# Kernel tuning notes

Measured on AMD Instinct MI355X. Metric: run time of the kernel, lower is better.

Reference implementation:

```python
import jax, jax.numpy as jnp
import numpy as np

T = 2048          # total (flattened) tokens
HID = 4096
NQ = 32           # query heads
NKV = 8           # kv heads
D = 128           # head_dim
B = 4             # dllm block length (block-sparse attention block)
WIN = 1024        # sliding window
EPS = 1e-6


def _rope_tables():
    # standard RoPE cos/sin tables, half-dim frequencies duplicated
    inv_freq = 1.0 / (10000.0 ** (np.arange(0, D, 2, dtype=np.float32) / D))
    pos = np.arange(T, dtype=np.float32)
    freqs = np.outer(pos, inv_freq)                     # [T, D/2]
    emb = np.concatenate([freqs, freqs], axis=-1)       # [T, D]
    return jnp.asarray(np.cos(emb)), jnp.asarray(np.sin(emb))


def setup_inputs() -> dict:
    key = jax.random.key(0)
    ks = jax.random.split(key, 4)
    cos, sin = _rope_tables()
    return {
        "hidden_states": jax.random.normal(ks[0], (T, HID), jnp.float32),
        "cos": cos,
        "sin": sin,
        "w_qkv": jax.random.normal(ks[1], (HID, (NQ + 2 * NKV) * D), jnp.float32) * (HID ** -0.5),
        "q_norm_w": jnp.ones((D,), jnp.float32),
        "k_norm_w": jnp.ones((D,), jnp.float32),
        "w_o": jax.random.normal(ks[2], (NQ * D, HID), jnp.float32) * ((NQ * D) ** -0.5),
    }


def _rmsnorm(x, w):
    # per-head RMSNorm over last dim (head_dim)
    var = jnp.mean(jnp.square(x), axis=-1, keepdims=True)
    return x * jax.lax.rsqrt(var + EPS) * w


def _rotate_half(x):
    x1, x2 = jnp.split(x, 2, axis=-1)
    return jnp.concatenate([-x2, x1], axis=-1)


def reference(hidden_states, cos, sin, w_qkv, q_norm_w, k_norm_w, w_o):
    # fused QKV projection on flattened tokens [T, HID]
    qkv = hidden_states @ w_qkv                                  # [T, (NQ+2NKV)*D]
    q, k, v = jnp.split(qkv, [NQ * D, (NQ + NKV) * D], axis=-1)
    q = q.reshape(T, NQ, D)
    k = k.reshape(T, NKV, D)
    v = v.reshape(T, NKV, D)

    # per-head QK RMSNorm
    q = _rmsnorm(q, q_norm_w)
    k = _rmsnorm(k, k_norm_w)

    # RoPE
    c = cos[:, None, :]
    s = sin[:, None, :]
    q = q * c + _rotate_half(q) * s
    k = k * c + _rotate_half(k) * s

    # GQA: expand kv heads to query heads
    groups = NQ // NKV
    k = jnp.repeat(k, groups, axis=1)                            # [T, NQ, D]
    v = jnp.repeat(v, groups, axis=1)

    # block-sparse (dLLM block-causal) + sliding-window mask:
    # token q attends to token j iff block(j) <= block(q) (full bidirectional
    # attention within a dllm block, causal across blocks) AND j is within
    # the sliding window.
    pos = jnp.arange(T)
    qb = pos // B
    allowed = (qb[None, :] <= qb[:, None]) & ((pos[:, None] - pos[None, :]) < WIN)

    scale = D ** -0.5
    scores = jnp.einsum("qhd,khd->hqk", q, k) * scale            # [NQ, T, T]
    scores = jnp.where(allowed[None, :, :], scores, jnp.float32(-1e30))
    probs = jax.nn.softmax(scores, axis=-1)
    attn = jnp.einsum("hqk,khd->qhd", probs, v)                   # [T, NQ, D]

    out = attn.reshape(T, NQ * D) @ w_o                           # [T, HID]
    return out
```

## Files before the change

### kernel.cpp

```cpp
#include <hip/hip_runtime.h>
#include <hip/hip_bf16.h>

typedef unsigned short u16;
typedef __attribute__((ext_vector_type(8))) short bf16x8;
typedef __attribute__((ext_vector_type(4))) float f32x4;
typedef __attribute__((ext_vector_type(8))) u16 u16x8;
typedef __attribute__((ext_vector_type(4))) u16 u16x4;

#define T_SEQ 2048
#define HID 4096
#define NQ 32
#define NKV 8
#define DH 128
#define WIN 1024

__device__ __forceinline__ u16 f2bf(float f) {
  union { float f; unsigned int u; } v; v.f = f;
  unsigned int u = v.u;
  unsigned int r = (u + 0x7FFFu + ((u >> 16) & 1u)) >> 16;
  return (u16)r;
}
__device__ __forceinline__ float bf2f(u16 b) {
  union { unsigned int u; float f; } v; v.u = ((unsigned int)b) << 16;
  return v.f;
}

__device__ __forceinline__ void gload16(const void* g, void* l) {
  __builtin_amdgcn_global_load_lds(
      (const __attribute__((address_space(1))) unsigned int*)g,
      (__attribute__((address_space(3))) unsigned int*)l, 16, 0, 0);
}

__global__ __launch_bounds__(256) void f32_to_bf16(const float* __restrict__ in,
                                                   u16* __restrict__ out, int n) {
  int i = (blockIdx.x * 256 + threadIdx.x) * 8;
  if (i >= n) return;
  float4 a = *(const float4*)(in + i);
  float4 b = *(const float4*)(in + i + 4);
  u16x8 r;
  r[0] = f2bf(a.x); r[1] = f2bf(a.y); r[2] = f2bf(a.z); r[3] = f2bf(a.w);
  r[4] = f2bf(b.x); r[5] = f2bf(b.y); r[6] = f2bf(b.z); r[7] = f2bf(b.w);
  *(u16x8*)(out + i) = r;
}

__global__ __launch_bounds__(256) void transpose_f32_to_bf16(const float* __restrict__ in,
                                                             u16* __restrict__ out,
                                                             int R, int C) {
  __shared__ float tile[64][65];
  int c0 = blockIdx.x * 64, r0 = blockIdx.y * 64;
  int tx = threadIdx.x, ty = threadIdx.y;
#pragma unroll
  for (int i = 0; i < 64; i += 16) {
    float4 v = *(const float4*)(in + (size_t)(r0 + ty + i) * C + c0 + tx * 4);
    tile[ty + i][tx * 4 + 0] = v.x;
    tile[ty + i][tx * 4 + 1] = v.y;
    tile[ty + i][tx * 4 + 2] = v.z;
    tile[ty + i][tx * 4 + 3] = v.w;
  }
  __syncthreads();
#pragma unroll
  for (int i = 0; i < 64; i += 16) {
    u16x4 o;
#pragma unroll
    for (int j = 0; j < 4; ++j) o[j] = f2bf(tile[tx * 4 + j][ty + i]);
    *(u16x4*)(out + (size_t)(c0 + ty + i) * R + r0 + tx * 4) = o;
  }
}

__global__ __launch_bounds__(256) void v_transpose(const u16* __restrict__ Vn,
                                                   u16* __restrict__ Vt) {
  __shared__ u16 tile[64][68];
  int tx = threadIdx.x & 15, ty = threadIdx.x >> 4;
  int t0 = blockIdx.x * 64, dh0 = blockIdx.y * 64;
#pragma unroll
  for (int i = 0; i < 64; i += 16) {
    u16x4 v = *(const u16x4*)(Vn + (size_t)(t0 + ty + i) * 1024 + dh0 + tx * 4);
    tile[ty + i][tx * 4 + 0] = v[0];
    tile[ty + i][tx * 4 + 1] = v[1];
    tile[ty + i][tx * 4 + 2] = v[2];
    tile[ty + i][tx * 4 + 3] = v[3];
  }
  __syncthreads();
#pragma unroll
  for (int i = 0; i < 64; i += 16) {
    u16x4 o;
#pragma unroll
    for (int j = 0; j < 4; ++j) o[j] = tile[tx * 4 + j][ty + i];
    *(u16x4*)(Vt + (size_t)(dh0 + ty + i) * 2048 + t0 + tx * 4) = o;
  }
}

template <int NF, bool BF16OUT>
__global__ __launch_bounds__(512, 2) void gemm_1w(const u16* __restrict__ A,
                                                  const u16* __restrict__ Bt,
                                                  void* __restrict__ Cv,
                                                  int N, int K, int NT) {
  constexpr int HN = NF * 16;
  constexpr int BN = 4 * HN;
  constexpr int NB = BN / 64;
  __shared__ u16 lsA[2][16384];
  __shared__ u16 lsB[3][BN * 64];
  const int tid = threadIdx.x;
  const int lane = tid & 63, w = tid >> 6;
  const int wm = w >> 1, wn = w & 1;
  const int l15 = lane & 15, l4 = lane >> 4;

  const int nwg = gridDim.x;
  const int cpx = nwg >> 3;
  const int bid = blockIdx.x;
  const int swz = (bid & 7) * cpx + (bid >> 3);
  const int bm = (swz & 7) * 256;
  const int bn = (swz >> 3) * BN;

  auto stageA = [&](int unit, int slot, int kt) {
    int r = tid >> 3, cp = tid & 7;
    int scp = cp ^ (r & 7);
    gload16(A + (size_t)(bm + unit * 64 + r) * K + kt * 64 + scp * 8,
            (char*)lsA[slot] + (unit * 512 + tid) * 16);
  };
  auto stageB = [&](int unit, int slot, int kt) {
    int r = tid >> 3, cp = tid & 7;
    int scp = cp ^ (r & 7);
    gload16(Bt + (size_t)(bn + unit * 64 + r) * K + kt * 64 + scp * 8,
            (char*)lsB[slot] + (unit * 512 + tid) * 16);
  };
  auto rdA = [&](int slot, int mf, int ks) -> bf16x8 {
    int r = wm * 64 + mf * 16 + l15;
    int ch = (ks * 4 + l4) ^ (r & 7);
    return *(const bf16x8*)(lsA[slot] + r * 64 + ch * 8);
  };
  auto rdB = [&](int slot, int nf, int ks) -> bf16x8 {
    int r = wn * 2 * HN + nf * 16 + l15;
    int ch = (ks * 4 + l4) ^ (r & 7);
    return *(const bf16x8*)(lsB[slot] + r * 64 + ch * 8);
  };

#define WAIT_NB() do { if constexpr (NB == 3) asm volatile("s_waitcnt vmcnt(3)" ::: "memory"); \
                       else                   asm volatile("s_waitcnt vmcnt(2)" ::: "memory"); } while (0)

  f32x4 acc[4][2 * NF] = {};
  bf16x8 afA[4][2], bfr[2 * NF][2];

  stageA(0, 0, 0); stageA(1, 0, 0); stageA(2, 0, 0); stageA(3, 0, 0);
#pragma unroll
  for (int u = 0; u < NB; ++u) stageB(u, 0, 0);
#pragma unroll
  for (int u = 0; u < NB; ++u) stageB(u, 1, 1);
  WAIT_NB();
  __builtin_amdgcn_s_barrier();

  for (int t = 0; t < NT; ++t) {
    const int sA = t & 1, sB = t % 3;
    const int ktA = (t + 1 < NT) ? t + 1 : NT - 1;
    const int ktB = (t + 2 < NT) ? t + 2 : NT - 1;

#pragma unroll
    for (int mf = 0; mf < 4; ++mf)
#pragma unroll
      for (int ks = 0; ks < 2; ++ks) afA[mf][ks] = rdA(sA, mf, ks);
#pragma unroll
    for (int nf = 0; nf < 2 * NF; ++nf)
#pragma unroll
      for (int ks = 0; ks < 2; ++ks) bfr[nf][ks] = rdB(sB, nf, ks);
    stageA(0, (t + 1) & 1, ktA); stageA(1, (t + 1) & 1, ktA);
    stageA(2, (t + 1) & 1, ktA); stageA(3, (t + 1) & 1, ktA);
#pragma unroll
    for (int u = 0; u < NB; ++u) stageB(u, (t + 2) % 3, ktB);
    __builtin_amdgcn_s_setprio(1);
#pragma unroll
    for (int nf = 0; nf < 2 * NF; ++nf)
#pragma unroll
      for (int mf = 0; mf < 4; ++mf) {
        acc[mf][nf] = __builtin_amdgcn_mfma_f32_16x16x32_bf16(afA[mf][0], bfr[nf][0], acc[mf][nf], 0, 0, 0);
        acc[mf][nf] = __builtin_amdgcn_mfma_f32_16x16x32_bf16(afA[mf][1], bfr[nf][1], acc[mf][nf], 0, 0, 0);
      }
    __builtin_amdgcn_s_setprio(0);
    asm volatile("s_waitcnt lgkmcnt(0)" ::: "memory");
    WAIT_NB();
    __builtin_amdgcn_s_barrier();
  }

  asm volatile("s_waitcnt vmcnt(0)" ::: "memory");

#pragma unroll
  for (int mi = 0; mi < 4; ++mi)
#pragma unroll
    for (int ni = 0; ni < 2 * NF; ++ni) {
      int row = bm + wm * 64 + mi * 16 + l4 * 4;
      int col = bn + wn * 2 * HN + ni * 16 + l15;
      if constexpr (BF16OUT) {
        u16* dst = (u16*)Cv;
#pragma unroll
        for (int j = 0; j < 4; ++j)
          dst[(size_t)(row + j) * N + col] = f2bf(acc[mi][ni][j]);
      } else {
        float* p = (float*)Cv + (size_t)row * N + col;
        p[0] = acc[mi][ni][0];
        p[(size_t)N] = acc[mi][ni][1];
        p[2 * (size_t)N] = acc[mi][ni][2];
        p[3 * (size_t)N] = acc[mi][ni][3];
      }
    }
#undef WAIT_NB
}

__global__ __launch_bounds__(256, 2) void gemm_1wh(const u16* __restrict__ A,
                                                   const u16* __restrict__ Bt,
                                                   float* __restrict__ C,
                                                   int N, int K, int NT) {
  __shared__ u16 lsA[2][8192];
  __shared__ u16 lsB[3][8192];
  const int tid = threadIdx.x;
  const int lane = tid & 63, w = tid >> 6;
  const int wm = w >> 1, wn = w & 1;
  const int l15 = lane & 15, l4 = lane >> 4;

  const int nwg = gridDim.x;
  const int cpx = nwg >> 3;
  const int bid = blockIdx.x;
  const int swz = (bid & 7) * cpx + (bid >> 3);
  const int bm = (swz & 15) * 128;
  const int bn = (swz >> 4) * 128;

  auto stageA = [&](int unit, int slot, int kt) {
    int r = unit * 32 + (tid >> 3), cp = tid & 7;
    int scp = cp ^ (r & 7);
    gload16(A + (size_t)(bm + r) * K + kt * 64 + scp * 8,
            (char*)lsA[slot] + (unit * 256 + tid) * 16);
  };
  auto stageB = [&](int unit, int slot, int kt) {
    int r = unit * 32 + (tid >> 3), cp = tid & 7;
    int scp = cp ^ (r & 7);
    gload16(Bt + (size_t)(bn + r) * K + kt * 64 + scp * 8,
            (char*)lsB[slot] + (unit * 256 + tid) * 16);
  };
  auto rdA = [&](int slot, int mf, int ks) -> bf16x8 {
    int r = wm * 64 + mf * 16 + l15;
    int ch = (ks * 4 + l4) ^ (r & 7);
    return *(const bf16x8*)(lsA[slot] + r * 64 + ch * 8);
  };
  auto rdB = [&](int slot, int nf, int ks) -> bf16x8 {
    int r = wn * 64 + nf * 16 + l15;
    int ch = (ks * 4 + l4) ^ (r & 7);
    return *(const bf16x8*)(lsB[slot] + r * 64 + ch * 8);
  };

  f32x4 acc[4][4] = {};
  bf16x8 afA[4][2], bfr[4][2];

#pragma unroll
  for (int u = 0; u < 4; ++u) stageA(u, 0, 0);
#pragma unroll
  for (int u = 0; u < 4; ++u) stageB(u, 0, 0);
#pragma unroll
  for (int u = 0; u < 4; ++u) stageB(u, 1, 1);
  asm volatile("s_waitcnt vmcnt(4)" ::: "memory");
  __builtin_amdgcn_s_barrier();

  for (int t = 0; t < NT; ++t) {
    const int sA = t & 1, sB = t % 3;
    const int ktA = (t + 1 < NT) ? t + 1 : NT - 1;
    const int ktB = (t + 2 < NT) ? t + 2 : NT - 1;

#pragma unroll
    for (int mf = 0; mf < 4; ++mf)
#pragma unroll
      for (int ks = 0; ks < 2; ++ks) afA[mf][ks] = rdA(sA, mf, ks);
#pragma unroll
    for (int nf = 0; nf < 4; ++nf)
#pragma unroll
      for (int ks = 0; ks < 2; ++ks) bfr[nf][ks] = rdB(sB, nf, ks);
#pragma unroll
    for (int u = 0; u < 4; ++u) stageA(u, (t + 1) & 1, ktA);
#pragma unroll
    for (int u = 0; u < 4; ++u) stageB(u, (t + 2) % 3, ktB);
    __builtin_amdgcn_s_setprio(1);
#pragma unroll
    for (int nf = 0; nf < 4; ++nf)
#pragma unroll
      for (int mf = 0; mf < 4; ++mf) {
        acc[mf][nf] = __builtin_amdgcn_mfma_f32_16x16x32_bf16(afA[mf][0], bfr[nf][0], acc[mf][nf], 0, 0, 0);
        acc[mf][nf] = __builtin_amdgcn_mfma_f32_16x16x32_bf16(afA[mf][1], bfr[nf][1], acc[mf][nf], 0, 0, 0);
      }
    __builtin_amdgcn_s_setprio(0);
    asm volatile("s_waitcnt lgkmcnt(0)" ::: "memory");
    asm volatile("s_waitcnt vmcnt(4)" ::: "memory");
    __builtin_amdgcn_s_barrier();
  }

  asm volatile("s_waitcnt vmcnt(0)" ::: "memory");

#pragma unroll
  for (int mi = 0; mi < 4; ++mi)
#pragma unroll
    for (int ni = 0; ni < 4; ++ni) {
      int row = bm + wm * 64 + mi * 16 + l4 * 4;
      int col = bn + wn * 64 + ni * 16 + l15;
      float* p = C + (size_t)row * N + col;
      p[0] = acc[mi][ni][0];
      p[(size_t)N] = acc[mi][ni][1];
      p[2 * (size_t)N] = acc[mi][ni][2];
      p[3 * (size_t)N] = acc[mi][ni][3];
    }
}

__global__ __launch_bounds__(256) void rope_kernel(const u16* __restrict__ qkv,
                                                   const float* __restrict__ cosb,
                                                   const float* __restrict__ sinb,
                                                   const float* __restrict__ qw,
                                                   const float* __restrict__ kw,
                                                   u16* __restrict__ Qo,
                                                   u16* __restrict__ Ko,
                                                   u16* __restrict__ Vn) {
  const int tid = threadIdx.x;
  const int v = blockIdx.x * 16 + (tid >> 4);
  const int j = tid & 15;
  const int t = v / 48, hid = v % 48;
  u16x8 raw = *(const u16x8*)(qkv + (size_t)v * 128 + j * 8);
  if (hid < NQ + NKV) {
    float xf[8];
    float ss = 0.f;
#pragma unroll
    for (int i = 0; i < 8; ++i) { xf[i] = bf2f(raw[i]); ss += xf[i] * xf[i]; }
    ss += __shfl_xor(ss, 1); ss += __shfl_xor(ss, 2);
    ss += __shfl_xor(ss, 4); ss += __shfl_xor(ss, 8);
    float inv = rsqrtf(ss * (1.0f / 128.0f) + 1e-6f);
    const float* wn = (hid < NQ) ? qw : kw;
    float4 w0 = *(const float4*)(wn + j * 8);
    float4 w1 = *(const float4*)(wn + j * 8 + 4);
    float wv[8] = {w0.x, w0.y, w0.z, w0.w, w1.x, w1.y, w1.z, w1.w};
    float n[8], p[8];
#pragma unroll
    for (int i = 0; i < 8; ++i) n[i] = xf[i] * inv * wv[i];
#pragma unroll
    for (int i = 0; i < 8; ++i) p[i] = __shfl_xor(n[i], 8);
    const float sgn = (j < 8) ? -1.f : 1.f;
    const float* cb = cosb + t * 128 + j * 8;
    const float* sb = sinb + t * 128 + j * 8;
    float4 c0 = *(const float4*)cb, c1 = *(const float4*)(cb + 4);
    float4 s0 = *(const float4*)sb, s1 = *(const float4*)(sb + 4);
    float cc[8] = {c0.x, c0.y, c0.z, c0.w, c1.x, c1.y, c1.z, c1.w};
    float sv[8] = {s0.x, s0.y, s0.z, s0.w, s1.x, s1.y, s1.z, s1.w};
    const float scale = (hid < NQ) ? 0.08838834764831845f * 1.44269504088896341f : 1.0f;
    u16x8 o;
#pragma unroll
    for (int i = 0; i < 8; ++i)
      o[i] = f2bf((n[i] * cc[i] + sgn * p[i] * sv[i]) * scale);
    if (hid < NQ)
      *(u16x8*)(Qo + ((size_t)hid * T_SEQ + t) * 128 + j * 8) = o;
    else
      *(u16x8*)(Ko + ((size_t)(hid - NQ) * T_SEQ + t) * 128 + j * 8) = o;
  } else {
    *(u16x8*)(Vn + (size_t)t * 1024 + (hid - (NQ + NKV)) * 128 + j * 8) = raw;
  }
}

__global__ __launch_bounds__(256) void attn_kernel(const u16* __restrict__ Q,
                                                   const u16* __restrict__ Kb,
                                                   const u16* __restrict__ Vt,
                                                   u16* __restrict__ O) {
  __shared__ u16 kls[2][64 * 128];
  __shared__ u16 vls[2][128 * 64];
  __shared__ u16 plds[4][16 * 72];

  const int tid = threadIdx.x;
  const int lane = tid & 63, w = tid >> 6;
  const int l15 = lane & 15, l4 = lane >> 4;
  const int h = blockIdx.x;
  const int q0 = blockIdx.y * 64;
  const int wq0 = q0 + w * 16;
  const int kvh = h >> 2;

  bf16x8 qf[4];
  {
    const u16* qrow = Q + ((size_t)h * T_SEQ + (wq0 + l15)) * DH;
    for (int ks = 0; ks < 4; ++ks)
      qf[ks] = *(const bf16x8*)(qrow + ks * 32 + l4 * 8);
  }

  f32x4 acc[8] = {};
  float m = -1e30f, lsum = 0.f;

  int ks0 = q0 - (WIN - 1); if (ks0 < 0) ks0 = 0;
  ks0 &= ~63;
  const int kend = q0;

  auto stage = [&](int b, int k0) {
#pragma unroll
    for (int c = 0; c < 4; ++c) {
      int base = w * 4096 + c * 1024;
      int idx = base / 16 + lane;
      {
        int row = idx >> 4;
        int col = (idx & 15) ^ (row & 7);
        gload16(Kb + ((size_t)kvh * T_SEQ + k0 + row) * DH + col * 8,
                (char*)kls[b] + base);
      }
      {
        int d = idx >> 3;
        int ch = (idx & 7) ^ (d & 7);
        gload16(Vt + ((size_t)kvh * DH + d) * T_SEQ + k0 + ch * 8,
                (char*)vls[b] + base);
      }
    }
  };

  stage(0, ks0);
  int buf = 0;
  for (int k0 = ks0; k0 <= kend; k0 += 64) {
    bool more = (k0 + 64 <= kend);
    if (more) stage(buf ^ 1, k0 + 64);
    if (more) { asm volatile("s_waitcnt vmcnt(8)" ::: "memory"); }
    else      { asm volatile("s_waitcnt vmcnt(0)" ::: "memory"); }
    __builtin_amdgcn_s_barrier();

    if (k0 <= wq0 + 15 && k0 + 63 >= wq0 - (WIN - 1)) {
      f32x4 st[4];
      __builtin_amdgcn_s_setprio(1);
#pragma unroll
      for (int kh = 0; kh < 4; ++kh) {
        f32x4 s = {};
        int row = kh * 16 + l15;
        const char* kb = (const char*)kls[buf] + row * 256;
#pragma unroll
        for (int ks = 0; ks < 4; ++ks) {
          int chunk = (ks * 4 + l4) ^ (row & 7);
          bf16x8 kf = *(const bf16x8*)(kb + chunk * 16);
          s = __builtin_amdgcn_mfma_f32_16x16x32_bf16(kf, qf[ks], s, 0, 0, 0);
        }
        st[kh] = s;
      }
      __builtin_amdgcn_s_setprio(0);
      const int q = wq0 + l15;
      float pv[4][4];
      float mx = -3e38f;
      if (k0 + 64 <= wq0 && k0 >= wq0 - 1008) {
#pragma unroll
        for (int kh = 0; kh < 4; ++kh)
#pragma unroll
          for (int i = 0; i < 4; ++i) {
            pv[kh][i] = st[kh][i];
            mx = fmaxf(mx, pv[kh][i]);
          }
      } else {
#pragma unroll
        for (int kh = 0; kh < 4; ++kh)
#pragma unroll
          for (int i = 0; i < 4; ++i) {
            int k = k0 + kh * 16 + l4 * 4 + i;
            bool ok = ((k >> 2) <= (q >> 2)) && (q - k < WIN);
            float s = ok ? st[kh][i] : -3e38f;
            pv[kh][i] = s;
            mx = fmaxf(mx, s);
          }
      }
      mx = fmaxf(mx, __shfl_xor(mx, 16));
      mx = fmaxf(mx, __shfl_xor(mx, 32));
      if (!__all(mx <= m + 11.5f)) {
        float mn = fmaxf(m, mx);
        float sc = __builtin_amdgcn_exp2f(m - mn);
        m = mn;
        lsum *= sc;
#pragma unroll
        for (int nt = 0; nt < 8; ++nt)
#pragma unroll
          for (int i = 0; i < 4; ++i) acc[nt][i] *= sc;
      }
      float rs = 0.f;
#pragma unroll
      for (int kh = 0; kh < 4; ++kh)
#pragma unroll
        for (int i = 0; i < 4; ++i) {
          float p = __builtin_amdgcn_exp2f(pv[kh][i] - m);
          pv[kh][i] = p;
          rs += p;
        }
      rs += __shfl_xor(rs, 16);
      rs += __shfl_xor(rs, 32);
      lsum += rs;
      u16* pw = plds[w];
#pragma unroll
      for (int kh = 0; kh < 4; ++kh) {
        unsigned int d0, d1;
        asm("v_cvt_pk_bf16_f32 %0, %1, %2" : "=v"(d0) : "v"(pv[kh][0]), "v"(pv[kh][1]));
        asm("v_cvt_pk_bf16_f32 %0, %1, %2" : "=v"(d1) : "v"(pv[kh][2]), "v"(pv[kh][3]));
        *(unsigned int*)(pw + l15 * 72 + kh * 16 + l4 * 4) = d0;
        *(unsigned int*)(pw + l15 * 72 + kh * 16 + l4 * 4 + 2) = d1;
      }
      bf16x8 pf0 = *(const bf16x8*)(pw + l15 * 72 + l4 * 8);
      bf16x8 pf1 = *(const bf16x8*)(pw + l15 * 72 + 32 + l4 * 8);
      __builtin_amdgcn_s_setprio(1);
#pragma unroll
      for (int nt = 0; nt < 8; ++nt) {
        int d = nt * 16 + l15;
        int ch0 = l4 ^ (d & 7);
        int ch1 = (4 + l4) ^ (d & 7);
        bf16x8 vf0 = *(const bf16x8*)((const char*)vls[buf] + d * 128 + ch0 * 16);
        bf16x8 vf1 = *(const bf16x8*)((const char*)vls[buf] + d * 128 + ch1 * 16);
        acc[nt] = __builtin_amdgcn_mfma_f32_16x16x32_bf16(vf0, pf0, acc[nt], 0, 0, 0);
        acc[nt] = __builtin_amdgcn_mfma_f32_16x16x32_bf16(vf1, pf1, acc[nt], 0, 0, 0);
      }
      __builtin_amdgcn_s_setprio(0);
    }
    __builtin_amdgcn_s_barrier();
    buf ^= 1;
  }

  float inv = 1.0f / lsum;
#pragma unroll
  for (int nt = 0; nt < 8; ++nt) {
    u16x4 o;
#pragma unroll
    for (int i = 0; i < 4; ++i) o[i] = f2bf(acc[nt][i] * inv);
    *(u16x4*)(O + (size_t)(wq0 + l15) * (NQ * DH) + h * DH + nt * 16 + l4 * 4) = o;
  }
}

extern "C" void kernel_launch(void* const* d_in, const int* in_sizes, int n_in,
                              void* d_out, int out_size, void* d_ws, size_t ws_size,
                              hipStream_t stream) {
  const float* hidden = (const float*)d_in[0];
  const float* cosb   = (const float*)d_in[1];
  const float* sinb   = (const float*)d_in[2];
  const float* w_qkv  = (const float*)d_in[3];
  const float* qnw    = (const float*)d_in[4];
  const float* knw    = (const float*)d_in[5];
  const float* w_o    = (const float*)d_in[6];
  float* out = (float*)d_out;
  char* ws = (char*)d_ws;

  u16*   wqkvT  = (u16*)(ws);
  u16*   hid_bf = (u16*)(ws + ((size_t)48 << 20));
  u16*   qkv_bf = (u16*)(ws + ((size_t)64 << 20));
  u16*   vn_bf  = (u16*)(ws + ((size_t)88 << 20));
  u16*   q_bf   = (u16*)(ws + ((size_t)112 << 20));
  u16*   k_bf   = (u16*)(ws + ((size_t)128 << 20));
  u16*   vt_bf  = (u16*)(ws + ((size_t)132 << 20));
  u16*   attn_bf= (u16*)(ws + ((size_t)48 << 20));
  u16*   woT    = (u16*)(ws);

  f32_to_bf16<<<4096, 256, 0, stream>>>(hidden, hid_bf, T_SEQ * HID);
  transpose_f32_to_bf16<<<dim3(96, 64), dim3(16, 16), 0, stream>>>(w_qkv, wqkvT, HID, 6144);
  gemm_1w<3, true><<<256, 512, 0, stream>>>(hid_bf, wqkvT, qkv_bf, 6144, HID, 64);
  transpose_f32_to_bf16<<<dim3(64, 64), dim3(16, 16), 0, stream>>>(w_o, woT, NQ * DH, HID);
  rope_kernel<<<(T_SEQ * 48) / 16, 256, 0, stream>>>(qkv_bf, cosb, sinb, qnw, knw, q_bf, k_bf, vn_bf);
  v_transpose<<<dim3(32, 16), 256, 0, stream>>>(vn_bf, vt_bf);
  attn_kernel<<<dim3(NQ, T_SEQ / 64), 256, 0, stream>>>(q_bf, k_bf, vt_bf, attn_bf);
  gemm_1wh<<<512, 256, 0, stream>>>(attn_bf, woT, out, HID, NQ * DH, 64);
}
```

Measured before the change: 295.3 us.

## Give each attention wave two 16-row query tiles, halving waves per block

```diff
diff --git a/kernel.cpp b/kernel.cpp
--- a/kernel.cpp
+++ b/kernel.cpp
@@ -355,31 +355,33 @@
   }
 }
 
-__global__ __launch_bounds__(256) void attn_kernel(const u16* __restrict__ Q,
+__global__ __launch_bounds__(128) void attn_kernel(const u16* __restrict__ Q,
                                                    const u16* __restrict__ Kb,
                                                    const u16* __restrict__ Vt,
                                                    u16* __restrict__ O) {
   __shared__ u16 kls[2][64 * 128];
   __shared__ u16 vls[2][128 * 64];
-  __shared__ u16 plds[4][16 * 72];
+  __shared__ u16 plds[2][2][16 * 72];
 
   const int tid = threadIdx.x;
   const int lane = tid & 63, w = tid >> 6;
   const int l15 = lane & 15, l4 = lane >> 4;
   const int h = blockIdx.x;
   const int q0 = blockIdx.y * 64;
-  const int wq0 = q0 + w * 16;
+  const int wq0 = q0 + w * 32;
   const int kvh = h >> 2;
 
-  bf16x8 qf[4];
-  {
-    const u16* qrow = Q + ((size_t)h * T_SEQ + (wq0 + l15)) * DH;
+  bf16x8 qf[2][4];
+#pragma unroll
+  for (int qh = 0; qh < 2; ++qh) {
+    const u16* qrow = Q + ((size_t)h * T_SEQ + (wq0 + qh * 16 + l15)) * DH;
+#pragma unroll
     for (int ks = 0; ks < 4; ++ks)
-      qf[ks] = *(const bf16x8*)(qrow + ks * 32 + l4 * 8);
-  }
-
-  f32x4 acc[8] = {};
-  float m = -1e30f, lsum = 0.f;
+      qf[qh][ks] = *(const bf16x8*)(qrow + ks * 32 + l4 * 8);
+  }
+
+  f32x4 acc[2][8] = {};
+  float m[2] = {-1e30f, -1e30f}, lsum[2] = {0.f, 0.f};
 
   int ks0 = q0 - (WIN - 1); if (ks0 < 0) ks0 = 0;
   ks0 &= ~63;
@@ -387,8 +389,8 @@
 
   auto stage = [&](int b, int k0) {
 #pragma unroll
-    for (int c = 0; c < 4; ++c) {
-      int base = w * 4096 + c * 1024;
+    for (int c = 0; c < 8; ++c) {
+      int base = w * 8192 + c * 1024;
       int idx = base / 16 + lane;
       {
         int row = idx >> 4;
@@ -410,85 +412,94 @@
   for (int k0 = ks0; k0 <= kend; k0 += 64) {
     bool more = (k0 + 64 <= kend);
     if (more) stage(buf ^ 1, k0 + 64);
-    if (more) { asm volatile("s_waitcnt vmcnt(8)" ::: "memory"); }
+    if (more) { asm volatile("s_waitcnt vmcnt(16)" ::: "memory"); }
     else      { asm volatile("s_waitcnt vmcnt(0)" ::: "memory"); }
     __builtin_amdgcn_s_barrier();
 
-    if (k0 <= wq0 + 15 && k0 + 63 >= wq0 - (WIN - 1)) {
-      f32x4 st[4];
+    if (k0 <= wq0 + 31 && k0 + 63 >= wq0 - (WIN - 1)) {
+      f32x4 st[2][4];
       __builtin_amdgcn_s_setprio(1);
 #pragma unroll
       for (int kh = 0; kh < 4; ++kh) {
-        f32x4 s = {};
+        f32x4 s0 = {}, s1 = {};
         int row = kh * 16 + l15;
         const char* kb = (const char*)kls[buf] + row * 256;
 #pragma unroll
         for (int ks = 0; ks < 4; ++ks) {
           int chunk = (ks * 4 + l4) ^ (row & 7);
           bf16x8 kf = *(const bf16x8*)(kb + chunk * 16);
-          s = __builtin_amdgcn_mfma_f32_16x16x32_bf16(kf, qf[ks], s, 0, 0, 0);
+          s0 = __builtin_amdgcn_mfma_f32_16x16x32_bf16(kf, qf[0][ks], s0, 0, 0, 0);
+          s1 = __builtin_amdgcn_mfma_f32_16x16x32_bf16(kf, qf[1][ks], s1, 0, 0, 0);
         }
-        st[kh] = s;
+        st[0][kh] = s0; st[1][kh] = s1;
       }
       __builtin_amdgcn_s_setprio(0);
-      const int q = wq0 + l15;
-      float pv[4][4];
-      float mx = -3e38f;
-      if (k0 + 64 <= wq0 && k0 >= wq0 - 1008) {
+#pragma unroll
+      for (int qh = 0; qh < 2; ++qh) {
+        const int wqq = wq0 + qh * 16;
+        const int q = wqq + l15;
+        float pv[4][4];
+        float mx = -3e38f;
+        if (k0 + 64 <= wqq && k0 >= wqq - 1008) {
+#pragma unroll
+          for (int kh = 0; kh < 4; ++kh)
+#pragma unroll
+            for (int i = 0; i < 4; ++i) {
+              pv[kh][i] = st[qh][kh][i];
+              mx = fmaxf(mx, pv[kh][i]);
+            }
+        } else {
+#pragma unroll
+          for (int kh = 0; kh < 4; ++kh)
+#pragma unroll
+            for (int i = 0; i < 4; ++i) {
+              int k = k0 + kh * 16 + l4 * 4 + i;
+              bool ok = ((k >> 2) <= (q >> 2)) && (q - k < WIN);
+              float s = ok ? st[qh][kh][i] : -3e38f;
+              pv[kh][i] = s;
+              mx = fmaxf(mx, s);
+            }
+        }
+        mx = fmaxf(mx, __shfl_xor(mx, 16));
+        mx = fmaxf(mx, __shfl_xor(mx, 32));
+        if (!__all(mx <= m[qh] + 11.5f)) {
+          float mn = fmaxf(m[qh], mx);
+          float sc = __builtin_amdgcn_exp2f(m[qh] - mn);
+          m[qh] = mn;
+          lsum[qh] *= sc;
+#pragma unroll
+          for (int nt = 0; nt < 8; ++nt)
+#pragma unroll
+            for (int i = 0; i < 4; ++i) acc[qh][nt][i] *= sc;
+        }
+        float rs = 0.f;
 #pragma unroll
         for (int kh = 0; kh < 4; ++kh)
 #pragma unroll
           for (int i = 0; i < 4; ++i) {
-            pv[kh][i] = st[kh][i];
-            mx = fmaxf(mx, pv[kh][i]);
+            float p = __builtin_amdgcn_exp2f(pv[kh][i] - m[qh]);
+            pv[kh][i] = p;
+            rs += p;
           }
-      } else {
-#pragma unroll
-        for (int kh = 0; kh < 4; ++kh)
-#pragma unroll
-          for (int i = 0; i < 4; ++i) {
-            int k = k0 + kh * 16 + l4 * 4 + i;
-            bool ok = ((k >> 2) <= (q >> 2)) && (q - k < WIN);
-            float s = ok ? st[kh][i] : -3e38f;
-            pv[kh][i] = s;
-            mx = fmaxf(mx, s);
-          }
-      }
-      mx = fmaxf(mx, __shfl_xor(mx, 16));
-      mx = fmaxf(mx, __shfl_xor(mx, 32));
-      if (!__all(mx <= m + 11.5f)) {
-        float mn = fmaxf(m, mx);
-        float sc = __builtin_amdgcn_exp2f(m - mn);
-        m = mn;
-        lsum *= sc;
-#pragma unroll
-        for (int nt = 0; nt < 8; ++nt)
-#pragma unroll
-          for (int i = 0; i < 4; ++i) acc[nt][i] *= sc;
-      }
-      float rs = 0.f;
-#pragma unroll
-      for (int kh = 0; kh < 4; ++kh)
-#pragma unroll
-        for (int i = 0; i < 4; ++i) {
-          float p = __builtin_amdgcn_exp2f(pv[kh][i] - m);
-          pv[kh][i] = p;
-          rs += p;
+        rs += __shfl_xor(rs, 16);
+        rs += __shfl_xor(rs, 32);
+        lsum[qh] += rs;
+        u16* pw = plds[w][qh];
+#pragma unroll
+        for (int kh = 0; kh < 4; ++kh) {
+          unsigned int d0, d1;
+          asm("v_cvt_pk_bf16_f32 %0, %1, %2" : "=v"(d0) : "v"(pv[kh][0]), "v"(pv[kh][1]));
+          asm("v_cvt_pk_bf16_f32 %0, %1, %2" : "=v"(d1) : "v"(pv[kh][2]), "v"(pv[kh][3]));
+          *(unsigned int*)(pw + l15 * 72 + kh * 16 + l4 * 4) = d0;
+          *(unsigned int*)(pw + l15 * 72 + kh * 16 + l4 * 4 + 2) = d1;
         }
-      rs += __shfl_xor(rs, 16);
-      rs += __shfl_xor(rs, 32);
-      lsum += rs;
-      u16* pw = plds[w];
-#pragma unroll
-      for (int kh = 0; kh < 4; ++kh) {
-        unsigned int d0, d1;
-        asm("v_cvt_pk_bf16_f32 %0, %1, %2" : "=v"(d0) : "v"(pv[kh][0]), "v"(pv[kh][1]));
-        asm("v_cvt_pk_bf16_f32 %0, %1, %2" : "=v"(d1) : "v"(pv[kh][2]), "v"(pv[kh][3]));
-        *(unsigned int*)(pw + l15 * 72 + kh * 16 + l4 * 4) = d0;
-        *(unsigned int*)(pw + l15 * 72 + kh * 16 + l4 * 4 + 2) = d1;
-      }
-      bf16x8 pf0 = *(const bf16x8*)(pw + l15 * 72 + l4 * 8);
-      bf16x8 pf1 = *(const bf16x8*)(pw + l15 * 72 + 32 + l4 * 8);
+      }
+      bf16x8 pf[2][2];
+#pragma unroll
+      for (int qh = 0; qh < 2; ++qh) {
+        pf[qh][0] = *(const bf16x8*)(plds[w][qh] + l15 * 72 + l4 * 8);
+        pf[qh][1] = *(const bf16x8*)(plds[w][qh] + l15 * 72 + 32 + l4 * 8);
+      }
       __builtin_amdgcn_s_setprio(1);
 #pragma unroll
       for (int nt = 0; nt < 8; ++nt) {
@@ -497,8 +508,10 @@
         int ch1 = (4 + l4) ^ (d & 7);
         bf16x8 vf0 = *(const bf16x8*)((const char*)vls[buf] + d * 128 + ch0 * 16);
         bf16x8 vf1 = *(const bf16x8*)((const char*)vls[buf] + d * 128 + ch1 * 16);
-        acc[nt] = __builtin_amdgcn_mfma_f32_16x16x32_bf16(vf0, pf0, acc[nt], 0, 0, 0);
-        acc[nt] = __builtin_amdgcn_mfma_f32_16x16x32_bf16(vf1, pf1, acc[nt], 0, 0, 0);
+        acc[0][nt] = __builtin_amdgcn_mfma_f32_16x16x32_bf16(vf0, pf[0][0], acc[0][nt], 0, 0, 0);
+        acc[0][nt] = __builtin_amdgcn_mfma_f32_16x16x32_bf16(vf1, pf[0][1], acc[0][nt], 0, 0, 0);
+        acc[1][nt] = __builtin_amdgcn_mfma_f32_16x16x32_bf16(vf0, pf[1][0], acc[1][nt], 0, 0, 0);
+        acc[1][nt] = __builtin_amdgcn_mfma_f32_16x16x32_bf16(vf1, pf[1][1], acc[1][nt], 0, 0, 0);
       }
       __builtin_amdgcn_s_setprio(0);
     }
@@ -506,13 +519,16 @@
     buf ^= 1;
   }
 
-  float inv = 1.0f / lsum;
-#pragma unroll
-  for (int nt = 0; nt < 8; ++nt) {
-    u16x4 o;
-#pragma unroll
-    for (int i = 0; i < 4; ++i) o[i] = f2bf(acc[nt][i] * inv);
-    *(u16x4*)(O + (size_t)(wq0 + l15) * (NQ * DH) + h * DH + nt * 16 + l4 * 4) = o;
+#pragma unroll
+  for (int qh = 0; qh < 2; ++qh) {
+    float inv = 1.0f / lsum[qh];
+#pragma unroll
+    for (int nt = 0; nt < 8; ++nt) {
+      u16x4 o;
+#pragma unroll
+      for (int i = 0; i < 4; ++i) o[i] = f2bf(acc[qh][nt][i] * inv);
+      *(u16x4*)(O + (size_t)(wq0 + qh * 16 + l15) * (NQ * DH) + h * DH + nt * 16 + l4 * 4) = o;
+    }
   }
 }
 
@@ -545,6 +561,6 @@
   transpose_f32_to_bf16<<<dim3(64, 64), dim3(16, 16), 0, stream>>>(w_o, woT, NQ * DH, HID);
   rope_kernel<<<(T_SEQ * 48) / 16, 256, 0, stream>>>(qkv_bf, cosb, sinb, qnw, knw, q_bf, k_bf, vn_bf);
   v_transpose<<<dim3(32, 16), 256, 0, stream>>>(vn_bf, vt_bf);
-  attn_kernel<<<dim3(NQ, T_SEQ / 64), 256, 0, stream>>>(q_bf, k_bf, vt_bf, attn_bf);
+  attn_kernel<<<dim3(NQ, T_SEQ / 64), 128, 0, stream>>>(q_bf, k_bf, vt_bf, attn_bf);
   gemm_1wh<<<512, 256, 0, stream>>>(attn_bf, woT, out, HID, NQ * DH, 64);
 }
```

Result: slower. 308.9 us (+4.6%).

## Replace QKV GEMM with 128x128-tile kernel using 256 threads and 768 workgroups

Applied to the files above, without the earlier changes.

```diff
diff --git a/kernel.cpp b/kernel.cpp
--- a/kernel.cpp
+++ b/kernel.cpp
@@ -88,6 +88,105 @@
     for (int j = 0; j < 4; ++j) o[j] = tile[tx * 4 + j][ty + i];
     *(u16x4*)(Vt + (size_t)(dh0 + ty + i) * 2048 + t0 + tx * 4) = o;
   }
+}
+
+template <bool BF16OUT>
+__global__ __launch_bounds__(256, 3) void gemm_hw(const u16* __restrict__ A,
+                                                  const u16* __restrict__ Bt,
+                                                  void* __restrict__ Cv,
+                                                  int N, int K, int NT) {
+  __shared__ u16 lsA[2][4096];
+  __shared__ u16 lsB[3][4096];
+  const int tid = threadIdx.x;
+  const int lane = tid & 63, w = tid >> 6;
+  const int wm = w >> 1, wn = w & 1;
+  const int l15 = lane & 15, l4 = lane >> 4;
+
+  const int nwg = gridDim.x;
+  const int cpx = nwg >> 3;
+  const int bid = blockIdx.x;
+  const int swz = (bid & 7) * cpx + (bid >> 3);
+  const int bm = (swz & 15) * 128;
+  const int bn = (swz >> 4) * 128;
+
+  auto stageA = [&](int unit, int slot, int kt) {
+    int c = unit * 256 + tid;
+    int r = c >> 2, cp = c & 3;
+    int scp = cp ^ ((r >> 1) & 3);
+    gload16(A + (size_t)(bm + r) * K + kt * 32 + scp * 8,
+            (char*)lsA[slot] + c * 16);
+  };
+  auto stageB = [&](int unit, int slot, int kt) {
+    int c = unit * 256 + tid;
+    int r = c >> 2, cp = c & 3;
+    int scp = cp ^ ((r >> 1) & 3);
+    gload16(Bt + (size_t)(bn + r) * K + kt * 32 + scp * 8,
+            (char*)lsB[slot] + c * 16);
+  };
+  auto rdA = [&](int slot, int mf) -> bf16x8 {
+    int r = wm * 64 + mf * 16 + l15;
+    int ch = l4 ^ ((r >> 1) & 3);
+    return *(const bf16x8*)(lsA[slot] + r * 32 + ch * 8);
+  };
+  auto rdB = [&](int slot, int nf) -> bf16x8 {
+    int r = wn * 64 + nf * 16 + l15;
+    int ch = l4 ^ ((r >> 1) & 3);
+    return *(const bf16x8*)(lsB[slot] + r * 32 + ch * 8);
+  };
+
+  f32x4 acc[4][4] = {};
+  bf16x8 afA[4], bfr[4];
+
+  stageA(0, 0, 0); stageA(1, 0, 0);
+  stageB(0, 0, 0); stageB(1, 0, 0);
+  stageB(0, 1, 1); stageB(1, 1, 1);
+  asm volatile("s_waitcnt vmcnt(2)" ::: "memory");
+  __builtin_amdgcn_s_barrier();
+
+  for (int t = 0; t < NT; ++t) {
+    const int sA = t & 1, sB = t % 3;
+    const int ktA = (t + 1 < NT) ? t + 1 : NT - 1;
+    const int ktB = (t + 2 < NT) ? t + 2 : NT - 1;
+
+#pragma unroll
+    for (int mf = 0; mf < 4; ++mf) afA[mf] = rdA(sA, mf);
+#pragma unroll
+    for (int nf = 0; nf < 4; ++nf) bfr[nf] = rdB(sB, nf);
+    stageA(0, (t + 1) & 1, ktA); stageA(1, (t + 1) & 1, ktA);
+    stageB(0, (t + 2) % 3, ktB); stageB(1, (t + 2) % 3, ktB);
+    __builtin_amdgcn_s_setprio(1);
+#pragma unroll
+    for (int nf = 0; nf < 4; ++nf)
+#pragma unroll
+      for (int mf = 0; mf < 4; ++mf)
+        acc[mf][nf] = __builtin_amdgcn_mfma_f32_16x16x32_bf16(afA[mf], bfr[nf], acc[mf][nf], 0, 0, 0);
+    __builtin_amdgcn_s_setprio(0);
+    asm volatile("s_waitcnt lgkmcnt(0)" ::: "memory");
+    asm volatile("s_waitcnt vmcnt(2)" ::: "memory");
+    __builtin_amdgcn_s_barrier();
+  }
+
+  asm volatile("s_waitcnt vmcnt(0)" ::: "memory");
+
+#pragma unroll
+  for (int mi = 0; mi < 4; ++mi)
+#pragma unroll
+    for (int ni = 0; ni < 4; ++ni) {
+      int row = bm + wm * 64 + mi * 16 + l4 * 4;
+      int col = bn + wn * 64 + ni * 16 + l15;
+      if constexpr (BF16OUT) {
+        u16* dst = (u16*)Cv;
+#pragma unroll
+        for (int j = 0; j < 4; ++j)
+          dst[(size_t)(row + j) * N + col] = f2bf(acc[mi][ni][j]);
+      } else {
+        float* p = (float*)Cv + (size_t)row * N + col;
+        p[0] = acc[mi][ni][0];
+        p[(size_t)N] = acc[mi][ni][1];
+        p[2 * (size_t)N] = acc[mi][ni][2];
+        p[3 * (size_t)N] = acc[mi][ni][3];
+      }
+    }
 }
 
 template <int NF, bool BF16OUT>
@@ -541,7 +640,7 @@
 
   f32_to_bf16<<<4096, 256, 0, stream>>>(hidden, hid_bf, T_SEQ * HID);
   transpose_f32_to_bf16<<<dim3(96, 64), dim3(16, 16), 0, stream>>>(w_qkv, wqkvT, HID, 6144);
-  gemm_1w<3, true><<<256, 512, 0, stream>>>(hid_bf, wqkvT, qkv_bf, 6144, HID, 64);
+  gemm_hw<true><<<768, 256, 0, stream>>>(hid_bf, wqkvT, qkv_bf, 6144, HID, 128);
   transpose_f32_to_bf16<<<dim3(64, 64), dim3(16, 16), 0, stream>>>(w_o, woT, NQ * DH, HID);
   rope_kernel<<<(T_SEQ * 48) / 16, 256, 0, stream>>>(qkv_bf, cosb, sinb, qnw, knw, q_bf, k_bf, vn_bf);
   v_transpose<<<dim3(32, 16), 256, 0, stream>>>(vn_bf, vt_bf);
```

Result: slower. 320.1 us (+8.4%).
